# Optimization experiments

Hardware: AMD Instinct MI355X
Metric: run time of the kernel (lower is better)

The kernel has to match this reference:

```python
import jax, jax.numpy as jnp
import numpy as np

HEADS = 4
DIM_HEAD = 64
DIM = 256
FMAP = 64
SCALE = DIM_HEAD ** -0.5


def setup_inputs() -> dict:
    key = jax.random.key(0)
    k1, k2, k3, k4 = jax.random.split(key, 4)
    inner = HEADS * DIM_HEAD
    fmap = jax.random.normal(k1, (4, DIM, FMAP, FMAP), dtype=jnp.float32)
    # 1x1 conv weight for qkv projection: (3*inner_dim, dim)
    w_qkv = jax.random.normal(k2, (3 * inner, DIM), dtype=jnp.float32) * (DIM ** -0.5)
    # AbsPosEmb parameters, initialized as randn * dim_head**-0.5 (as in BoTNet)
    pos_height = jax.random.normal(k3, (FMAP, DIM_HEAD), dtype=jnp.float32) * SCALE
    pos_width = jax.random.normal(k4, (FMAP, DIM_HEAD), dtype=jnp.float32) * SCALE
    return {"fmap": fmap, "w_qkv": w_qkv, "pos_height": pos_height, "pos_width": pos_width}


def reference(fmap, w_qkv, pos_height, pos_width):
    b, c, h, w = fmap.shape
    hw = h * w
    # 1x1 conv (no bias) == channel matmul
    qkv = jnp.einsum('bchw,oc->bohw', fmap, w_qkv)  # (b, 3*inner, h, w)
    q, k, v = jnp.split(qkv, 3, axis=1)
    # replicate torch .view(b, heads, h*w, -1): raw row-major reshape
    q = q.reshape(b, HEADS, hw, DIM_HEAD) * SCALE
    k = k.reshape(b, HEADS, hw, DIM_HEAD)
    v = v.reshape(b, HEADS, hw, DIM_HEAD)
    sim = jnp.einsum('bhid,bhjd->bhij', q, k)  # (b, heads, hw, hw)
    # absolute positional bias: emb[j] = height[y] + width[x], j = y*w + x
    emb = (pos_height[:, None, :] + pos_width[None, :, :]).reshape(hw, DIM_HEAD)
    sim = sim + jnp.einsum('bhid,jd->bhij', q, emb)
    attn = jax.nn.softmax(sim, axis=-1)
    out = jnp.einsum('bhij,bhjd->bhid', attn, v)  # (b, heads, hw, dim_head)
    # replicate torch .view(b, heads*dim_head, h, w): raw reshape
    return out.reshape(b, HEADS * DIM_HEAD, h, w)
```

## Files before the change

kernel.cpp:

```cpp
#include <hip/hip_runtime.h>


typedef float  f32x4  __attribute__((ext_vector_type(4)));
typedef __bf16 bf16x8 __attribute__((ext_vector_type(8)));
typedef __bf16 bf16x4 __attribute__((ext_vector_type(4)));

__device__ inline float fast_exp2(float x) {
#if __has_builtin(__builtin_amdgcn_exp2f)
  return __builtin_amdgcn_exp2f(x);
#else
  return exp2f(x);
#endif
}

__device__ inline void glds16(const __bf16* g, __bf16* l) {
  __builtin_amdgcn_global_load_lds(
      (const __attribute__((address_space(1))) void*)g,
      (__attribute__((address_space(3))) void*)l, 16, 0, 0);
}

__global__ __launch_bounds__(256) void w_cvt(
    const float* __restrict__ w, __bf16* __restrict__ wb)
{
  int idx = blockIdx.x * 256 + threadIdx.x;
  f32x4 v = ((const f32x4*)w)[idx];
  bf16x4 o; o[0]=(__bf16)v[0]; o[1]=(__bf16)v[1]; o[2]=(__bf16)v[2]; o[3]=(__bf16)v[3];
  ((bf16x4*)wb)[idx] = o;
}

__global__ __launch_bounds__(256) void qkv_proj(
    const float* __restrict__ fmap, const __bf16* __restrict__ wb,
    const float* __restrict__ ph,   const float* __restrict__ pw,
    __bf16* __restrict__ Qw, __bf16* __restrict__ Kw, __bf16* __restrict__ Vw)
{
  constexpr int LS = 264;
  __shared__ __bf16 Bs[32 * LS];
  const int tid  = threadIdx.x;
  const int wv   = tid >> 6;
  const int lane = tid & 63;
  const int quad = lane >> 4, l15 = lane & 15;
  const int n0 = blockIdx.x * 32;
  const int b  = blockIdx.y;

#pragma unroll
  for (int i = 0; i < 2; ++i) {
    int id = tid + i * 256;
    int ng = id & 7;
    int kg = id >> 3;
    const float* base = fmap + ((size_t)b * 256 + 4 * kg) * 4096 + n0 + 4 * ng;
    f32x4 v0 = *(const f32x4*)(base);
    f32x4 v1 = *(const f32x4*)(base + 4096);
    f32x4 v2 = *(const f32x4*)(base + 8192);
    f32x4 v3 = *(const f32x4*)(base + 12288);
#pragma unroll
    for (int j = 0; j < 4; ++j) {
      bf16x4 o; o[0]=(__bf16)v0[j]; o[1]=(__bf16)v1[j]; o[2]=(__bf16)v2[j]; o[3]=(__bf16)v3[j];
      *(bf16x4*)(&Bs[(4 * ng + j) * LS + 4 * kg]) = o;
    }
  }
  __syncthreads();

  for (int mt = 0; mt < 12; ++mt) {
    const int region = mt >> 2;
    const int obase  = (mt & 3) * 64;
    const __bf16* aptr = wb + (size_t)(mt * 64 + 16 * wv + l15) * 256 + 8 * quad;

    f32x4 acc[2] = {};
#pragma unroll
    for (int k0 = 0; k0 < 256; k0 += 32) {
      bf16x8 af = *(const bf16x8*)(aptr + k0);
      bf16x8 b0 = *(const bf16x8*)(&Bs[(l15)      * LS + k0 + 8 * quad]);
      bf16x8 b1 = *(const bf16x8*)(&Bs[(16 + l15) * LS + k0 + 8 * quad]);
      acc[0] = __builtin_amdgcn_mfma_f32_16x16x32_bf16(af, b0, acc[0], 0, 0, 0);
      acc[1] = __builtin_amdgcn_mfma_f32_16x16x32_bf16(af, b1, acc[1], 0, 0, 0);
    }

#pragma unroll
    for (int t = 0; t < 2; ++t) {
#pragma unroll
      for (int rr = 0; rr < 4; ++rr) {
        int oreg = obase + 16 * wv + 4 * quad + rr;
        int s    = n0 + 16 * t + l15;
        float val = acc[t][rr];
        size_t off = ((size_t)(b * 256 + oreg)) * 4096 + s;
        if (region == 0) {
          Qw[off] = (__bf16)(val * 0.18033688f);
        } else if (region == 1) {
          int g = oreg & 63;
          float bias = ph[g * 64 + (s & 63)] + pw[(s >> 6) * 64 + (s & 63)];
          Kw[off] = (__bf16)(val + bias);
        } else {
          Vw[off] = (__bf16)val;
        }
      }
    }
  }
}

__global__ __launch_bounds__(256) void v_transpose(
    const __bf16* __restrict__ Vw, __bf16* __restrict__ Vt)
{
  __shared__ __bf16 T[64 * 72];
  const int tid = threadIdx.x;
  const int j0  = blockIdx.x * 64;
  const int bh  = blockIdx.y;
  const __bf16* src = Vw + (size_t)bh * 262144;
#pragma unroll
  for (int i = 0; i < 2; ++i) {
    int id = tid + i * 256;
    int r = id >> 3, c = (id & 7) * 8;
    *(bf16x8*)(&T[r * 72 + c]) = *(const bf16x8*)(src + (size_t)(j0 + r) * 64 + c);
  }
  __syncthreads();
#pragma unroll
  for (int i = 0; i < 2; ++i) {
    int id = tid + i * 256;
    int d = id >> 3, jc = (id & 7) * 8;
    bf16x8 o;
#pragma unroll
    for (int z = 0; z < 8; ++z) o[z] = T[(jc + z) * 72 + d];
    *(bf16x8*)(Vt + ((size_t)bh * 64 + d) * 4096 + j0 + jc) = o;
  }
}

__global__ __launch_bounds__(256, 2) void flash_attn(
    const __bf16* __restrict__ Qg, const __bf16* __restrict__ Kg,
    const __bf16* __restrict__ Vtg, __bf16* __restrict__ OP0,
    float* __restrict__ lws, float* __restrict__ Og)
{
  __shared__ __bf16 Ks[2 * 128 * 64];
  __shared__ __bf16 Vs[2 * 128 * 64];
  const int tid  = threadIdx.x;
  const int wv   = tid >> 6;
  const int lane = tid & 63;
  const int quad = lane >> 4, l15 = lane & 15;
  const int bh = blockIdx.y;
  const int z  = blockIdx.z;
  const int iw = blockIdx.x * 256 + 64 * wv;
  const int jbase = z * 2048;
  const __bf16* Qb = Qg  + (size_t)bh * 262144;
  const __bf16* Kb = Kg  + (size_t)bh * 262144;
  const __bf16* Vb = Vtg + (size_t)bh * 262144;

  bf16x8 qf[4][2];
#pragma unroll
  for (int m = 0; m < 4; ++m)
#pragma unroll
    for (int c = 0; c < 2; ++c)
      qf[m][c] = *(const bf16x8*)(Qb + (size_t)(iw + 16 * m + l15) * 64 + 32 * c + 8 * quad);

  const int r0  = tid >> 3;
  const int kch = tid & 7;
  const int xc  = (kch ^ (r0 & 7)) * 8;
  const int pr0a = r0, pr1a = r0 + 32;
  const int pr0 = (pr0a & 0x23) | ((pr0a & 0x0C) << 1) | ((pr0a & 0x10) >> 2);
  const int pr1 = (pr1a & 0x23) | ((pr1a & 0x0C) << 1) | ((pr1a & 0x10) >> 2);
  const __bf16* kp0 = Kb + (size_t)(jbase + pr0) * 64 + xc;
  const __bf16* kp1 = Kb + (size_t)(jbase + pr1) * 64 + xc;
  const __bf16* vp0 = Vb + (size_t)r0 * 4096        + jbase + xc;
  const __bf16* vp1 = Vb + (size_t)(r0 + 32) * 4096 + jbase + xc;

  f32x4 acco[4][4] = {};
  f32x4 lacc[4] = {};
  const int swz = (l15 & 7);

  bf16x8 onesb;
#pragma unroll
  for (int r = 0; r < 8; ++r) onesb[r] = (__bf16)1.0f;

  auto dma_tile = [&](int buf) {
    __bf16* k0 = &Ks[buf * 8192 + tid * 8];
    __bf16* v0 = &Vs[buf * 8192 + tid * 8];
    glds16(kp0, k0);         kp0 += 4096;
    glds16(kp1, k0 + 2048);  kp1 += 4096;
    glds16(vp0, v0);         vp0 += 64;
    glds16(vp1, v0 + 2048);  vp1 += 64;
    glds16(kp0, k0 + 4096);  kp0 += 4096;
    glds16(kp1, k0 + 6144);  kp1 += 4096;
    glds16(vp0, v0 + 4096);  vp0 += 64;
    glds16(vp1, v0 + 6144);  vp1 += 64;
  };

  auto compute_tile = [&](int buf, int sub) {
    const __bf16* Kbuf = &Ks[buf * 8192 + sub * 4096];
    const __bf16* Vbuf = &Vs[buf * 8192 + sub * 4096];
    f32x4 sacc[4][4] = {};
    __builtin_amdgcn_s_setprio(1);
#pragma unroll
    for (int c = 0; c < 2; ++c) {
#pragma unroll
      for (int t = 0; t < 4; ++t) {
        bf16x8 ak = *(const bf16x8*)(&Kbuf[(16 * t + l15) * 64 + (((4 * c + quad) ^ swz) * 8)]);
#pragma unroll
        for (int m = 0; m < 4; ++m)
          sacc[m][t] = __builtin_amdgcn_mfma_f32_16x16x32_bf16(ak, qf[m][c], sacc[m][t], 0, 0, 0);
      }
    }
    __builtin_amdgcn_s_setprio(0);
    bf16x8 pf[4][2];
#pragma unroll
    for (int m = 0; m < 4; ++m) {
#pragma unroll
      for (int t = 0; t < 4; ++t)
#pragma unroll
        for (int r = 0; r < 4; ++r)
          sacc[m][t][r] = fast_exp2(sacc[m][t][r]);
#pragma unroll
      for (int c2 = 0; c2 < 2; ++c2) {
        bf16x8 a;
#pragma unroll
        for (int r = 0; r < 4; ++r) {
          a[r]     = (__bf16)sacc[m][2 * c2][r];
          a[4 + r] = (__bf16)sacc[m][2 * c2 + 1][r];
        }
        pf[m][c2] = a;
      }
    }
    __builtin_amdgcn_s_setprio(1);
#pragma unroll
    for (int c2 = 0; c2 < 2; ++c2) {
#pragma unroll
      for (int t = 0; t < 4; ++t) {
        bf16x8 bv = *(const bf16x8*)(&Vbuf[(16 * t + l15) * 64 + (((4 * c2 + quad) ^ swz) * 8)]);
#pragma unroll
        for (int m = 0; m < 4; ++m)
          acco[m][t] = __builtin_amdgcn_mfma_f32_16x16x32_bf16(pf[m][c2], bv, acco[m][t], 0, 0, 0);
      }
#pragma unroll
      for (int m = 0; m < 4; ++m)
        lacc[m] = __builtin_amdgcn_mfma_f32_16x16x32_bf16(pf[m][c2], onesb, lacc[m], 0, 0, 0);
    }
    __builtin_amdgcn_s_setprio(0);
  };

  dma_tile(0);
  for (int it = 0; it < 16; it += 2) {
    __syncthreads();
    dma_tile(1);
    compute_tile(0, 0);
    compute_tile(0, 1);
    __syncthreads();
    if (it < 14) dma_tile(0);
    compute_tile(1, 0);
    compute_tile(1, 1);
  }

#pragma unroll
  for (int m = 0; m < 4; ++m) {
    if (l15 == 0) {
#pragma unroll
      for (int r = 0; r < 4; ++r)
        lws[z * 65536 + bh * 4096 + iw + 16 * m + 4 * quad + r] = lacc[m][r];
    }
  }
  if (z == 0) {
    __bf16* Ob = OP0 + (size_t)bh * 262144;
#pragma unroll
    for (int m = 0; m < 4; ++m)
#pragma unroll
      for (int t = 0; t < 4; ++t)
#pragma unroll
        for (int r = 0; r < 4; ++r)
          Ob[(size_t)(iw + 16 * m + 4 * quad + r) * 64 + 16 * t + l15] =
              (__bf16)acco[m][t][r];
  } else {
    float* Ob = Og + (size_t)bh * 262144;
#pragma unroll
    for (int m = 0; m < 4; ++m)
#pragma unroll
      for (int t = 0; t < 4; ++t)
#pragma unroll
        for (int r = 0; r < 4; ++r)
          Ob[(size_t)(iw + 16 * m + 4 * quad + r) * 64 + 16 * t + l15] =
              acco[m][t][r];
  }
}

__global__ __launch_bounds__(256) void combine(
    const __bf16* __restrict__ OP0, const float* __restrict__ lws,
    float* __restrict__ Og)
{
  int idx = blockIdx.x * 256 + threadIdx.x;
  int row = idx >> 4;
  float inv = 1.0f / (lws[row] + lws[65536 + row]);
  f32x4 o = ((const f32x4*)Og)[idx];
  bf16x4 p = ((const bf16x4*)OP0)[idx];
  f32x4 r;
#pragma unroll
  for (int k = 0; k < 4; ++k) r[k] = (o[k] + (float)p[k]) * inv;
  ((f32x4*)Og)[idx] = r;
}

extern "C" void kernel_launch(void* const* d_in, const int* in_sizes, int n_in,
                              void* d_out, int out_size, void* d_ws, size_t ws_size,
                              hipStream_t stream) {
  const float* fmap = (const float*)d_in[0];
  const float* w    = (const float*)d_in[1];
  const float* ph   = (const float*)d_in[2];
  const float* pw   = (const float*)d_in[3];
  float* out = (float*)d_out;

  __bf16* Qw = (__bf16*)d_ws;
  __bf16* Kw = Qw + 4194304;
  __bf16* Vw = Kw + 4194304;
  __bf16* Vt = Vw + 4194304;
  float*  lws = (float*)(Vt + 4194304);
  __bf16* Wb16 = (__bf16*)(lws + 131072);

  w_cvt      <<<dim3(192),       256, 0, stream>>>(w, Wb16);
  qkv_proj   <<<dim3(128, 4),    256, 0, stream>>>(fmap, Wb16, ph, pw, Qw, Kw, Vw);
  v_transpose<<<dim3(64, 16),    256, 0, stream>>>(Vw, Vt);
  flash_attn <<<dim3(16, 16, 2), 256, 0, stream>>>(Qw, Kw, Vt, Vw , lws, out);
  combine    <<<dim3(4096),      256, 0, stream>>>(Vw , lws, out);
}
```

Measured before the change: 177.1 us.

## Interleave QK, exp and PV of two sub-tiles to overlap MFMA with exp

Replaces the two sequential per-sub-tile compute calls with a single software-pipelined routine. The exp and bf16 conversion of the first sub-tile's scores is interleaved with the QK MFMAs of the second sub-tile, and the second sub-tile's exp is interleaved with the first sub-tile's PV MFMAs. The goal is to hide transcendental and conversion work under matrix-core work. In exchange, two score accumulator sets and two probability fragment sets are live at once, which raises register pressure and risks spills or lower occupancy.

```diff
diff --git a/kernel.cpp b/kernel.cpp
--- a/kernel.cpp
+++ b/kernel.cpp
@@ -181,55 +181,99 @@
     glds16(vp1, v0 + 6144);  vp1 += 64;
   };
 
-  auto compute_tile = [&](int buf, int sub) {
-    const __bf16* Kbuf = &Ks[buf * 8192 + sub * 4096];
-    const __bf16* Vbuf = &Vs[buf * 8192 + sub * 4096];
-    f32x4 sacc[4][4] = {};
+  auto compute_pair = [&](int buf) {
+    const __bf16* K0 = &Ks[buf * 8192];
+    const __bf16* K1 = K0 + 4096;
+    const __bf16* V0 = &Vs[buf * 8192];
+    const __bf16* V1 = V0 + 4096;
+    f32x4 s0[4][4] = {};
+    f32x4 s1[4][4] = {};
+    bf16x8 p0[4][2], p1[4][2];
+
     __builtin_amdgcn_s_setprio(1);
 #pragma unroll
-    for (int c = 0; c < 2; ++c) {
+    for (int c = 0; c < 2; ++c)
 #pragma unroll
       for (int t = 0; t < 4; ++t) {
-        bf16x8 ak = *(const bf16x8*)(&Kbuf[(16 * t + l15) * 64 + (((4 * c + quad) ^ swz) * 8)]);
+        bf16x8 ak = *(const bf16x8*)(&K0[(16 * t + l15) * 64 + (((4 * c + quad) ^ swz) * 8)]);
 #pragma unroll
         for (int m = 0; m < 4; ++m)
-          sacc[m][t] = __builtin_amdgcn_mfma_f32_16x16x32_bf16(ak, qf[m][c], sacc[m][t], 0, 0, 0);
-      }
-    }
+          s0[m][t] = __builtin_amdgcn_mfma_f32_16x16x32_bf16(ak, qf[m][c], s0[m][t], 0, 0, 0);
+      }
     __builtin_amdgcn_s_setprio(0);
-    bf16x8 pf[4][2];
-#pragma unroll
-    for (int m = 0; m < 4; ++m) {
+
+#pragma unroll
+    for (int u = 0; u < 4; ++u) {
+#pragma unroll
+      for (int c = 0; c < 2; ++c) {
+        bf16x8 ak = *(const bf16x8*)(&K1[(16 * u + l15) * 64 + (((4 * c + quad) ^ swz) * 8)]);
+#pragma unroll
+        for (int m = 0; m < 4; ++m)
+          s1[m][u] = __builtin_amdgcn_mfma_f32_16x16x32_bf16(ak, qf[m][c], s1[m][u], 0, 0, 0);
+      }
 #pragma unroll
       for (int t = 0; t < 4; ++t)
 #pragma unroll
         for (int r = 0; r < 4; ++r)
-          sacc[m][t][r] = fast_exp2(sacc[m][t][r]);
+          s0[u][t][r] = fast_exp2(s0[u][t][r]);
 #pragma unroll
       for (int c2 = 0; c2 < 2; ++c2) {
         bf16x8 a;
 #pragma unroll
         for (int r = 0; r < 4; ++r) {
-          a[r]     = (__bf16)sacc[m][2 * c2][r];
-          a[4 + r] = (__bf16)sacc[m][2 * c2 + 1][r];
+          a[r]     = (__bf16)s0[u][2 * c2][r];
+          a[4 + r] = (__bf16)s0[u][2 * c2 + 1][r];
         }
-        pf[m][c2] = a;
-      }
-    }
+        p0[u][c2] = a;
+      }
+    }
+
+#pragma unroll
+    for (int u = 0; u < 4; ++u) {
+#pragma unroll
+      for (int c2 = 0; c2 < 2; ++c2) {
+        bf16x8 bv = *(const bf16x8*)(&V0[(16 * u + l15) * 64 + (((4 * c2 + quad) ^ swz) * 8)]);
+#pragma unroll
+        for (int m = 0; m < 4; ++m)
+          acco[m][u] = __builtin_amdgcn_mfma_f32_16x16x32_bf16(p0[m][c2], bv, acco[m][u], 0, 0, 0);
+      }
+#pragma unroll
+      for (int t = 0; t < 4; ++t)
+#pragma unroll
+        for (int r = 0; r < 4; ++r)
+          s1[u][t][r] = fast_exp2(s1[u][t][r]);
+#pragma unroll
+      for (int c2 = 0; c2 < 2; ++c2) {
+        bf16x8 a;
+#pragma unroll
+        for (int r = 0; r < 4; ++r) {
+          a[r]     = (__bf16)s1[u][2 * c2][r];
+          a[4 + r] = (__bf16)s1[u][2 * c2 + 1][r];
+        }
+        p1[u][c2] = a;
+      }
+    }
+#pragma unroll
+    for (int c2 = 0; c2 < 2; ++c2)
+#pragma unroll
+      for (int m = 0; m < 4; ++m)
+        lacc[m] = __builtin_amdgcn_mfma_f32_16x16x32_bf16(p0[m][c2], onesb, lacc[m], 0, 0, 0);
+
     __builtin_amdgcn_s_setprio(1);
 #pragma unroll
-    for (int c2 = 0; c2 < 2; ++c2) {
-#pragma unroll
-      for (int t = 0; t < 4; ++t) {
-        bf16x8 bv = *(const bf16x8*)(&Vbuf[(16 * t + l15) * 64 + (((4 * c2 + quad) ^ swz) * 8)]);
+    for (int u = 0; u < 4; ++u)
+#pragma unroll
+      for (int c2 = 0; c2 < 2; ++c2) {
+        bf16x8 bv = *(const bf16x8*)(&V1[(16 * u + l15) * 64 + (((4 * c2 + quad) ^ swz) * 8)]);
 #pragma unroll
         for (int m = 0; m < 4; ++m)
-          acco[m][t] = __builtin_amdgcn_mfma_f32_16x16x32_bf16(pf[m][c2], bv, acco[m][t], 0, 0, 0);
-      }
+          acco[m][u] = __builtin_amdgcn_mfma_f32_16x16x32_bf16(p1[m][c2], bv, acco[m][u], 0, 0, 0);
+      }
+#pragma unroll
+    for (int c2 = 0; c2 < 2; ++c2)
 #pragma unroll
       for (int m = 0; m < 4; ++m)
-        lacc[m] = __builtin_amdgcn_mfma_f32_16x16x32_bf16(pf[m][c2], onesb, lacc[m], 0, 0, 0);
-    }
+        lacc[m] = __builtin_amdgcn_mfma_f32_16x16x32_bf16(p1[m][c2], onesb, lacc[m], 0, 0, 0);
     __builtin_amdgcn_s_setprio(0);
   };
 
@@ -237,12 +281,10 @@
   for (int it = 0; it < 16; it += 2) {
     __syncthreads();
     dma_tile(1);
-    compute_tile(0, 0);
-    compute_tile(0, 1);
+    compute_pair(0);
     __syncthreads();
     if (it < 14) dma_tile(0);
-    compute_tile(1, 0);
-    compute_tile(1, 1);
+    compute_pair(1);
   }
 
 #pragma unroll
```

Measured after the change: 185.4 us. +4.7%, slower.

## Merge split-K attention halves into one 512-thread block with LDS reduction

Applied to the files above, without the earlier changes.

The two key-range halves, previously separate blocks along grid z, now run as two groups of four waves inside a single 512-thread block. Each group stages its own K/V tiles in a shared 128KB LDS buffer. The groups then reduce their output and row-sum accumulators through LDS and write the normalized fp32 output directly. This removes the combine kernel, the bf16 partial-output and row-sum workspace round trips, and one launch. In exchange it doubles LDS per block, which may limit occupancy, and it adds a block-wide barrier epilogue.

```diff
diff --git a/kernel.cpp b/kernel.cpp
--- a/kernel.cpp
+++ b/kernel.cpp
@@ -123,21 +123,22 @@
   }
 }
 
-__global__ __launch_bounds__(256, 2) void flash_attn(
+__global__ __launch_bounds__(512, 2) void flash_attn(
     const __bf16* __restrict__ Qg, const __bf16* __restrict__ Kg,
-    const __bf16* __restrict__ Vtg, __bf16* __restrict__ OP0,
-    float* __restrict__ lws, float* __restrict__ Og)
+    const __bf16* __restrict__ Vtg, float* __restrict__ out)
 {
-  __shared__ __bf16 Ks[2 * 128 * 64];
-  __shared__ __bf16 Vs[2 * 128 * 64];
+  __shared__ __align__(16) __bf16 SMEM[65536];
+  __bf16* Ks = SMEM;
+  __bf16* Vs = SMEM + 32768;
+
   const int tid  = threadIdx.x;
   const int wv   = tid >> 6;
   const int lane = tid & 63;
   const int quad = lane >> 4, l15 = lane & 15;
+  const int zi   = wv >> 2;
+  const int wl   = wv & 3;
   const int bh = blockIdx.y;
-  const int z  = blockIdx.z;
-  const int iw = blockIdx.x * 256 + 64 * wv;
-  const int jbase = z * 2048;
+  const int iw = blockIdx.x * 256 + 64 * wl;
   const __bf16* Qb = Qg  + (size_t)bh * 262144;
   const __bf16* Kb = Kg  + (size_t)bh * 262144;
   const __bf16* Vb = Vtg + (size_t)bh * 262144;
@@ -152,13 +153,11 @@
   const int r0  = tid >> 3;
   const int kch = tid & 7;
   const int xc  = (kch ^ (r0 & 7)) * 8;
-  const int pr0a = r0, pr1a = r0 + 32;
-  const int pr0 = (pr0a & 0x23) | ((pr0a & 0x0C) << 1) | ((pr0a & 0x10) >> 2);
-  const int pr1 = (pr1a & 0x23) | ((pr1a & 0x0C) << 1) | ((pr1a & 0x10) >> 2);
-  const __bf16* kp0 = Kb + (size_t)(jbase + pr0) * 64 + xc;
-  const __bf16* kp1 = Kb + (size_t)(jbase + pr1) * 64 + xc;
-  const __bf16* vp0 = Vb + (size_t)r0 * 4096        + jbase + xc;
-  const __bf16* vp1 = Vb + (size_t)(r0 + 32) * 4096 + jbase + xc;
+  const int prr = (r0 & 0x23) | ((r0 & 0x0C) << 1) | ((r0 & 0x10) >> 2);
+  const __bf16* kp0 = Kb + (size_t)prr * 64 + xc;
+  const __bf16* kp1 = Kb + (size_t)(2048 + prr) * 64 + xc;
+  const __bf16* vp0 = Vb + (size_t)r0 * 4096 + xc;
+  const __bf16* vp1 = Vb + (size_t)r0 * 4096 + 2048 + xc;
 
   f32x4 acco[4][4] = {};
   f32x4 lacc[4] = {};
@@ -169,21 +168,23 @@
   for (int r = 0; r < 8; ++r) onesb[r] = (__bf16)1.0f;
 
   auto dma_tile = [&](int buf) {
-    __bf16* k0 = &Ks[buf * 8192 + tid * 8];
-    __bf16* v0 = &Vs[buf * 8192 + tid * 8];
-    glds16(kp0, k0);         kp0 += 4096;
-    glds16(kp1, k0 + 2048);  kp1 += 4096;
-    glds16(vp0, v0);         vp0 += 64;
-    glds16(vp1, v0 + 2048);  vp1 += 64;
-    glds16(kp0, k0 + 4096);  kp0 += 4096;
-    glds16(kp1, k0 + 6144);  kp1 += 4096;
-    glds16(vp0, v0 + 4096);  vp0 += 64;
-    glds16(vp1, v0 + 6144);  vp1 += 64;
+    __bf16* kd0 = &Ks[buf * 8192 + tid * 8];
+    __bf16* kd1 = &Ks[16384 + buf * 8192 + tid * 8];
+    __bf16* vd0 = &Vs[buf * 8192 + tid * 8];
+    __bf16* vd1 = &Vs[16384 + buf * 8192 + tid * 8];
+    glds16(kp0, kd0);         kp0 += 4096;
+    glds16(kp0, kd0 + 4096);  kp0 += 4096;
+    glds16(kp1, kd1);         kp1 += 4096;
+    glds16(kp1, kd1 + 4096);  kp1 += 4096;
+    glds16(vp0, vd0);         vp0 += 64;
+    glds16(vp0, vd0 + 4096);  vp0 += 64;
+    glds16(vp1, vd1);         vp1 += 64;
+    glds16(vp1, vd1 + 4096);  vp1 += 64;
   };
 
   auto compute_tile = [&](int buf, int sub) {
-    const __bf16* Kbuf = &Ks[buf * 8192 + sub * 4096];
-    const __bf16* Vbuf = &Vs[buf * 8192 + sub * 4096];
+    const __bf16* Kbuf = &Ks[zi * 16384 + buf * 8192 + sub * 4096];
+    const __bf16* Vbuf = &Vs[zi * 16384 + buf * 8192 + sub * 4096];
     f32x4 sacc[4][4] = {};
     __builtin_amdgcn_s_setprio(1);
 #pragma unroll
@@ -245,50 +246,39 @@
     compute_tile(1, 1);
   }
 
-#pragma unroll
-  for (int m = 0; m < 4; ++m) {
-    if (l15 == 0) {
-#pragma unroll
-      for (int r = 0; r < 4; ++r)
-        lws[z * 65536 + bh * 4096 + iw + 16 * m + 4 * quad + r] = lacc[m][r];
-    }
-  }
-  if (z == 0) {
-    __bf16* Ob = OP0 + (size_t)bh * 262144;
-#pragma unroll
-    for (int m = 0; m < 4; ++m)
+  __syncthreads();
+  float* X = (float*)SMEM;
+  const int slot = (wl * 64 + lane) * 84;
+  if (zi == 1) {
+#pragma unroll
+    for (int m = 0; m < 4; ++m) {
 #pragma unroll
       for (int t = 0; t < 4; ++t)
+        *(f32x4*)(&X[slot + m * 16 + t * 4]) = acco[m][t];
+      *(f32x4*)(&X[slot + 64 + m * 4]) = lacc[m];
+    }
+  }
+  __syncthreads();
+  if (zi == 0) {
+    float* Ob = out + (size_t)bh * 262144;
+#pragma unroll
+    for (int m = 0; m < 4; ++m) {
+      f32x4 l1 = *(const f32x4*)(&X[slot + 64 + m * 4]);
+      f32x4 lt = lacc[m] + l1;
+      f32x4 inv;
+#pragma unroll
+      for (int r = 0; r < 4; ++r) inv[r] = 1.0f / lt[r];
+#pragma unroll
+      for (int t = 0; t < 4; ++t) {
+        f32x4 o1 = *(const f32x4*)(&X[slot + m * 16 + t * 4]);
+        f32x4 ot = acco[m][t] + o1;
 #pragma unroll
         for (int r = 0; r < 4; ++r)
           Ob[(size_t)(iw + 16 * m + 4 * quad + r) * 64 + 16 * t + l15] =
-              (__bf16)acco[m][t][r];
-  } else {
-    float* Ob = Og + (size_t)bh * 262144;
-#pragma unroll
-    for (int m = 0; m < 4; ++m)
-#pragma unroll
-      for (int t = 0; t < 4; ++t)
-#pragma unroll
-        for (int r = 0; r < 4; ++r)
-          Ob[(size_t)(iw + 16 * m + 4 * quad + r) * 64 + 16 * t + l15] =
-              acco[m][t][r];
-  }
-}
-
-__global__ __launch_bounds__(256) void combine(
-    const __bf16* __restrict__ OP0, const float* __restrict__ lws,
-    float* __restrict__ Og)
-{
-  int idx = blockIdx.x * 256 + threadIdx.x;
-  int row = idx >> 4;
-  float inv = 1.0f / (lws[row] + lws[65536 + row]);
-  f32x4 o = ((const f32x4*)Og)[idx];
-  bf16x4 p = ((const bf16x4*)OP0)[idx];
-  f32x4 r;
-#pragma unroll
-  for (int k = 0; k < 4; ++k) r[k] = (o[k] + (float)p[k]) * inv;
-  ((f32x4*)Og)[idx] = r;
+              ot[r] * inv[r];
+      }
+    }
+  }
 }
 
 extern "C" void kernel_launch(void* const* d_in, const int* in_sizes, int n_in,
@@ -304,12 +294,10 @@
   __bf16* Kw = Qw + 4194304;
   __bf16* Vw = Kw + 4194304;
   __bf16* Vt = Vw + 4194304;
-  float*  lws = (float*)(Vt + 4194304);
-  __bf16* Wb16 = (__bf16*)(lws + 131072);
-
-  w_cvt      <<<dim3(192),       256, 0, stream>>>(w, Wb16);
-  qkv_proj   <<<dim3(128, 4),    256, 0, stream>>>(fmap, Wb16, ph, pw, Qw, Kw, Vw);
-  v_transpose<<<dim3(64, 16),    256, 0, stream>>>(Vw, Vt);
-  flash_attn <<<dim3(16, 16, 2), 256, 0, stream>>>(Qw, Kw, Vt, Vw , lws, out);
-  combine    <<<dim3(4096),      256, 0, stream>>>(Vw , lws, out);
-}
+  __bf16* Wb16 = Vt + 4194304;
+
+  w_cvt      <<<dim3(192),    256, 0, stream>>>(w, Wb16);
+  qkv_proj   <<<dim3(128, 4), 256, 0, stream>>>(fmap, Wb16, ph, pw, Qw, Kw, Vw);
+  v_transpose<<<dim3(64, 16), 256, 0, stream>>>(Vw, Vt);
+  flash_attn <<<dim3(16, 16), 512, 0, stream>>>(Qw, Kw, Vt, out);
+}
```

New measurement: 170.7 us. 3.6% less time.
